# Performance work log

Measured on AMD Instinct MI355X. Metric: run time of the kernel, lower is better.

## Reference

```python
import jax, jax.numpy as jnp
import numpy as np

H, N, CH, L = 256, 256, 1, 1024


def setup_inputs() -> dict:
    key = jax.random.key(0)
    k1, k2, k3, k4 = jax.random.split(key, 4)
    # Hurwitz-like A so the discretized dA is stable (|eig| < 1) over L powers
    A = 0.05 * jax.random.normal(k1, (H, N, N), jnp.float32) - jnp.eye(N, dtype=jnp.float32)
    B = jax.random.normal(k2, (H, N), jnp.float32)
    C = jax.random.normal(k3, (CH, H, N), jnp.float32)
    log_dt = jax.random.uniform(k4, (H,), jnp.float32,
                                minval=np.log(1e-3), maxval=np.log(1e-1))
    return {"A": A, "B": B, "C": C, "log_dt": log_dt}


def reference(A, B, C, log_dt):
    # Bilinear (Tustin) discretization:
    #   dA = (I - dt/2 A)^{-1} (I + dt/2 A),  dB = dt * (I - dt/2 A)^{-1} B
    dt = jnp.exp(log_dt)                                   # (H,)
    I = jnp.eye(A.shape[-1], dtype=A.dtype)
    A_bwd = I - (dt[:, None, None] / 2) * A                # (H, N, N)
    A_fwd = I + (dt[:, None, None] / 2) * A                # (H, N, N)
    dB = dt[:, None] * jnp.linalg.solve(A_bwd, B[..., None])[..., 0]   # (H, N)
    dA = jnp.linalg.solve(A_bwd, A_fwd)                    # (H, N, N)

    # Krylov kernel: k[c,h,l] = C[c,h,:] @ dA^l @ dB[h,:]
    def step(x, _):
        y = jnp.einsum('chn,hn->ch', C, x)                 # contract with C
        x_next = jnp.einsum('hmn,hn->hm', dA, x)           # advance state
        return x_next, y

    _, ys = jax.lax.scan(step, dB, None, length=L)         # ys: (L, CH, H)
    k = jnp.transpose(ys, (1, 2, 0))                       # (CH, H, L)
    return k
```

## Files before the change

kernel.cpp:

```cpp
#include <hip/hip_runtime.h>
#include <cstdint>
#include <cstddef>

#define NH 256
#define ND 256
#define NL 1024
#define NUV 16
#define NWV 64

typedef __attribute__((ext_vector_type(4))) float f32x4;
typedef __attribute__((ext_vector_type(8))) short short8;
typedef __attribute__((ext_vector_type(8))) unsigned short u16x8;
typedef __attribute__((ext_vector_type(4))) unsigned short u16x4;
typedef __attribute__((ext_vector_type(4))) unsigned int u32x4;

__device__ __forceinline__ float bfrec(unsigned short hi, unsigned short lo) {
  return __uint_as_float(((unsigned)hi) << 16) + __uint_as_float(((unsigned)lo) << 16);
}
__device__ __forceinline__ unsigned rne16(unsigned u) {
  return u + 0x7FFFu + ((u >> 16) & 1u);
}
__device__ __forceinline__ void bfsplit(float x, unsigned short& hi, unsigned short& lo) {
  unsigned u = __float_as_uint(x);
  unsigned r1 = rne16(u);
  hi = (unsigned short)(r1 >> 16);
  float lf = x - __uint_as_float(r1 & 0xFFFF0000u);
  unsigned r2 = rne16(__float_as_uint(lf));
  lo = (unsigned short)(r2 >> 16);
}
__device__ __forceinline__ void gload16(const void* g, void* l) {
  __builtin_amdgcn_global_load_lds(
      (const __attribute__((address_space(1))) unsigned int*)g,
      (__attribute__((address_space(3))) unsigned int*)l, 16, 0, 0);
}
__device__ __forceinline__ int ksw(int row) { return (row >> 1) & 3; }

__global__ __launch_bounds__(256) void prep_kernel(
    const float* __restrict__ A, const float* __restrict__ log_dt,
    unsigned short* __restrict__ Mhi, unsigned short* __restrict__ Mlo)
{
  size_t e0 = ((size_t)blockIdx.x * 256 + threadIdx.x) * 16;
  int h = (int)(e0 >> 16);
  float hdt = 0.5f * __expf(log_dt[h]);
  unsigned short hb[16], lb[16];
#pragma unroll
  for (int i = 0; i < 4; ++i) {
    f32x4 v = *(const f32x4*)(A + e0 + i * 4);
#pragma unroll
    for (int j = 0; j < 4; ++j) bfsplit(v[j] * hdt, hb[i * 4 + j], lb[i * 4 + j]);
  }
  unsigned ph[8], pl[8];
#pragma unroll
  for (int i = 0; i < 8; ++i) {
    ph[i] = (unsigned)hb[2 * i] | ((unsigned)hb[2 * i + 1] << 16);
    pl[i] = (unsigned)lb[2 * i] | ((unsigned)lb[2 * i + 1] << 16);
  }
  u32x4 a0 = {ph[0], ph[1], ph[2], ph[3]}, a1 = {ph[4], ph[5], ph[6], ph[7]};
  u32x4 b0 = {pl[0], pl[1], pl[2], pl[3]}, b1 = {pl[4], pl[5], pl[6], pl[7]};
  *(u32x4*)(Mhi + e0) = a0; *(u32x4*)(Mhi + e0 + 8) = a1;
  *(u32x4*)(Mlo + e0) = b0; *(u32x4*)(Mlo + e0 + 8) = b1;
}

template <int YT, int ADDX, int OUTN, int OUTT, int QOUT>
__global__ __launch_bounds__(256) void gemm128_kernel(
    const unsigned short* __restrict__ Xhi, const unsigned short* __restrict__ Xlo,
    const unsigned short* __restrict__ Yhi, const unsigned short* __restrict__ Ylo,
    unsigned short* __restrict__ Dhi, unsigned short* __restrict__ Dlo,
    unsigned short* __restrict__ DThi, unsigned short* __restrict__ DTlo,
    unsigned short* __restrict__ Qhi, unsigned short* __restrict__ Qlo)
{
  __shared__ unsigned short lds[33792];
  int tid = threadIdx.x;
  int lane = tid & 63, w = tid >> 6;
  int bid = blockIdx.x;
  int h = bid & 255, part = bid >> 8;
  int m0 = (part >> 1) * 128, n0 = (part & 1) * 128;
  size_t mb = (size_t)h * 65536;

  f32x4 acc[2][8];
#pragma unroll
  for (int m = 0; m < 2; ++m)
#pragma unroll
    for (int n = 0; n < 8; ++n) { f32x4 z = {0.f, 0.f, 0.f, 0.f}; acc[m][n] = z; }

  auto STAGE = [&](int s, int kb) {
#pragma unroll
    for (int j = 0; j < 2; ++j) {
      int c = j * 256 + tid;
      if (YT) {
        int row = c >> 2, sp = c & 3;
        int koff = kb * 32 + ((sp ^ ksw(row)) << 3);
        size_t gx = mb + (size_t)(m0 + row) * 256 + koff;
        size_t gy = mb + (size_t)(n0 + row) * 256 + koff;
        gload16(Xhi + gx, &lds[s * 8192 + c * 8]);
        gload16(Xlo + gx, &lds[s * 8192 + 4096 + c * 8]);
        gload16(Yhi + gy, &lds[16384 + s * 8192 + c * 8]);
        gload16(Ylo + gy, &lds[16384 + s * 8192 + 4096 + c * 8]);
      } else {
        {
          int row = c >> 2, sp = c & 3;
          size_t go = mb + (size_t)(m0 + row) * 256 + kb * 32 + ((sp ^ ksw(row)) << 3);
          gload16(Xhi + go, &lds[s * 8192 + c * 8]);
          gload16(Xlo + go, &lds[s * 8192 + 4096 + c * 8]);
        }
        {
          int k = c >> 4, ns = c & 15;
          size_t go = mb + (size_t)(kb * 32 + k) * 256 + n0 + ns * 8;
          gload16(Yhi + go, &lds[16384 + s * 8192 + c * 8]);
          gload16(Ylo + go, &lds[16384 + s * 8192 + 4096 + c * 8]);
        }
      }
    }
  };

  STAGE(0, 0);
  __builtin_amdgcn_sched_barrier(0);

  int nn = tid & 127, kh = tid >> 7;
  int cur = 0;
  for (int kb = 0; kb < 8; ++kb) {
    int nxt = cur ^ 1;
    if (kb < 7) {
      STAGE(nxt, kb + 1);
      __builtin_amdgcn_sched_barrier(0);
      asm volatile("s_waitcnt vmcnt(8)" ::: "memory");
    } else {
      asm volatile("s_waitcnt vmcnt(0)" ::: "memory");
    }
    __builtin_amdgcn_sched_barrier(0);
    __builtin_amdgcn_s_barrier();
    __builtin_amdgcn_sched_barrier(0);

    unsigned short* yb = &lds[16384 + cur * 8192];
    if (!YT) {
      unsigned short rh[16], rl[16];
#pragma unroll
      for (int i = 0; i < 16; ++i) {
        rh[i] = yb[(kh * 16 + i) * 128 + nn];
        rl[i] = yb[4096 + (kh * 16 + i) * 128 + nn];
      }
      asm volatile("s_waitcnt lgkmcnt(0)" ::: "memory");
      __builtin_amdgcn_sched_barrier(0);
      __builtin_amdgcn_s_barrier();
      __builtin_amdgcn_sched_barrier(0);
#pragma unroll
      for (int s2 = 0; s2 < 2; ++s2) {
        int sl = kh * 2 + s2;
        int off = nn * 32 + ((sl ^ ksw(nn)) << 3);
        u16x8 vh, vl;
#pragma unroll
        for (int e = 0; e < 8; ++e) { vh[e] = rh[s2 * 8 + e]; vl[e] = rl[s2 * 8 + e]; }
        *(u16x8*)&yb[off] = vh;
        *(u16x8*)&yb[4096 + off] = vl;
      }
      asm volatile("s_waitcnt lgkmcnt(0)" ::: "memory");
      __builtin_amdgcn_sched_barrier(0);
      __builtin_amdgcn_s_barrier();
      __builtin_amdgcn_sched_barrier(0);
    }

    int kg = lane >> 4, li = lane & 15;
    const unsigned short* xb = &lds[cur * 8192];
    short8 bhi[8], blo[8];
#pragma unroll
    for (int n = 0; n < 8; ++n) {
      int rowN = n * 16 + li;
      int off = rowN * 32 + ((kg ^ ksw(rowN)) << 3);
      bhi[n] = *(const short8*)&yb[off];
      blo[n] = *(const short8*)&yb[4096 + off];
    }
    __builtin_amdgcn_s_setprio(1);
#pragma unroll
    for (int m = 0; m < 2; ++m) {
      int rowM = w * 32 + m * 16 + li;
      int off = rowM * 32 + ((kg ^ ksw(rowM)) << 3);
      short8 ahi = *(const short8*)&xb[off];
      short8 alo = *(const short8*)&xb[4096 + off];
#pragma unroll
      for (int n = 0; n < 8; ++n) {
        acc[m][n] = __builtin_amdgcn_mfma_f32_16x16x32_bf16(ahi, bhi[n], acc[m][n], 0, 0, 0);
        acc[m][n] = __builtin_amdgcn_mfma_f32_16x16x32_bf16(ahi, blo[n], acc[m][n], 0, 0, 0);
        acc[m][n] = __builtin_amdgcn_mfma_f32_16x16x32_bf16(alo, bhi[n], acc[m][n], 0, 0, 0);
      }
    }
    __builtin_amdgcn_s_setprio(0);
    __builtin_amdgcn_sched_barrier(0);
    __builtin_amdgcn_s_barrier();
    __builtin_amdgcn_sched_barrier(0);
    cur = nxt;
  }

  float* fb = (float*)lds;
  {
    int q0 = (lane >> 4) * 4, li = lane & 15;
#pragma unroll
    for (int m = 0; m < 2; ++m)
#pragma unroll
      for (int n = 0; n < 8; ++n)
#pragma unroll
        for (int q = 0; q < 4; ++q)
          fb[(w * 32 + m * 16 + q0 + q) * 132 + n * 16 + li] = acc[m][n][q];
  }
  __syncthreads();
  if (OUTN || ADDX) {
    int row = tid >> 1, half = tid & 1;
#pragma unroll 1
    for (int hp = 0; hp < 2; ++hp) {
      int c0 = half * 64 + hp * 32;
      float v[32];
#pragma unroll
      for (int u = 0; u < 8; ++u) {
        f32x4 t4 = *(const f32x4*)&fb[row * 132 + c0 + u * 4];
#pragma unroll
        for (int e = 0; e < 4; ++e) v[u * 4 + e] = t4[e];
      }
      size_t go = mb + (size_t)(m0 + row) * 256 + n0 + c0;
      float xv[32];
      if (ADDX || QOUT) {
#pragma unroll
        for (int u = 0; u < 4; ++u) {
          u16x8 xh = *(const u16x8*)(Xhi + go + u * 8);
          u16x8 xl = *(const u16x8*)(Xlo + go + u * 8);
#pragma unroll
          for (int e = 0; e < 8; ++e) xv[u * 8 + e] = bfrec(xh[e], xl[e]);
        }
        if (ADDX) {
#pragma unroll
          for (int e = 0; e < 32; ++e) v[e] += xv[e];
          if (OUTT) {
#pragma unroll
            for (int u = 0; u < 8; ++u) {
              f32x4 t4;
#pragma unroll
              for (int e = 0; e < 4; ++e) t4[e] = v[u * 4 + e];
              *(f32x4*)&fb[row * 132 + c0 + u * 4] = t4;
            }
          }
        }
      }
      if (OUTN) {
        unsigned hw[16], lw[16];
#pragma unroll
        for (int i = 0; i < 16; ++i) {
          unsigned short ha, la, hb2, lb2;
          bfsplit(v[2 * i], ha, la);
          bfsplit(v[2 * i + 1], hb2, lb2);
          hw[i] = (unsigned)ha | ((unsigned)hb2 << 16);
          lw[i] = (unsigned)la | ((unsigned)lb2 << 16);
        }
#pragma unroll
        for (int u = 0; u < 4; ++u) {
          u32x4 a = {hw[u * 4], hw[u * 4 + 1], hw[u * 4 + 2], hw[u * 4 + 3]};
          u32x4 b = {lw[u * 4], lw[u * 4 + 1], lw[u * 4 + 2], lw[u * 4 + 3]};
          *(u32x4*)(Dhi + go + u * 8) = a;
          *(u32x4*)(Dlo + go + u * 8) = b;
        }
      }
      if (QOUT) {
        int grow = m0 + row, gc0 = n0 + c0;
        float qv[32];
#pragma unroll
        for (int e = 0; e < 32; ++e)
          qv[e] = v[e] + 2.f * xv[e] + ((gc0 + e) == grow ? 1.f : 0.f);
        unsigned hw[16], lw[16];
#pragma unroll
        for (int i = 0; i < 16; ++i) {
          unsigned short ha, la, hb2, lb2;
          bfsplit(qv[2 * i], ha, la);
          bfsplit(qv[2 * i + 1], hb2, lb2);
          hw[i] = (unsigned)ha | ((unsigned)hb2 << 16);
          lw[i] = (unsigned)la | ((unsigned)lb2 << 16);
        }
#pragma unroll
        for (int u = 0; u < 4; ++u) {
          u32x4 a = {hw[u * 4], hw[u * 4 + 1], hw[u * 4 + 2], hw[u * 4 + 3]};
          u32x4 b = {lw[u * 4], lw[u * 4 + 1], lw[u * 4 + 2], lw[u * 4 + 3]};
          *(u32x4*)(Qhi + go + u * 8) = a;
          *(u32x4*)(Qlo + go + u * 8) = b;
        }
      }
    }
  }
  if (OUTT) {
    if (ADDX) __syncthreads();
    int c = tid & 127, rh2 = tid >> 7;
#pragma unroll 1
    for (int ch2 = 0; ch2 < 2; ++ch2) {
      int r0 = rh2 * 64 + ch2 * 32;
      float tv[32];
#pragma unroll
      for (int i = 0; i < 32; ++i) tv[i] = fb[(r0 + i) * 132 + c];
      unsigned hw[16], lw[16];
#pragma unroll
      for (int i = 0; i < 16; ++i) {
        unsigned short ha, la, hb2, lb2;
        bfsplit(tv[2 * i], ha, la);
        bfsplit(tv[2 * i + 1], hb2, lb2);
        hw[i] = (unsigned)ha | ((unsigned)hb2 << 16);
        lw[i] = (unsigned)la | ((unsigned)lb2 << 16);
      }
      size_t go = mb + (size_t)(n0 + c) * 256 + m0 + r0;
#pragma unroll
      for (int u = 0; u < 4; ++u) {
        u32x4 a = {hw[u * 4], hw[u * 4 + 1], hw[u * 4 + 2], hw[u * 4 + 3]};
        u32x4 b = {lw[u * 4], lw[u * 4 + 1], lw[u * 4 + 2], lw[u * 4 + 3]};
        *(u32x4*)(DThi + go + u * 8) = a;
        *(u32x4*)(DTlo + go + u * 8) = b;
      }
    }
  }
}

__global__ __launch_bounds__(256) void db_kernel(
    const unsigned short* __restrict__ dAhi, const unsigned short* __restrict__ dAlo,
    const float* __restrict__ Bv, const float* __restrict__ log_dt, float* __restrict__ dB)
{
  int h = blockIdx.x, r = threadIdx.x;
  __shared__ float bl[256];
  bl[r] = Bv[h * 256 + r];
  __syncthreads();
  const unsigned short* ph = dAhi + (size_t)h * 65536 + (size_t)r * 256;
  const unsigned short* pl = dAlo + (size_t)h * 65536 + (size_t)r * 256;
  float acc = bl[r];
  for (int c8 = 0; c8 < 32; ++c8) {
    u16x8 vh = *(const u16x8*)(ph + c8 * 8);
    u16x8 vl = *(const u16x8*)(pl + c8 * 8);
#pragma unroll
    for (int e = 0; e < 8; ++e) acc += bfrec(vh[e], vl[e]) * bl[c8 * 8 + e];
  }
  dB[h * 256 + r] = 0.5f * __expf(log_dt[h]) * acc;
}

__device__ __forceinline__ int physc(int c) { return c + ((c >> 4) << 2); }

__global__ __launch_bounds__(1024) void chainAB_kernel(
    const unsigned short* __restrict__ UTh, const unsigned short* __restrict__ UTl,
    const unsigned short* __restrict__ Gh, const unsigned short* __restrict__ Gl,
    const float* __restrict__ Cin, const float* __restrict__ dB,
    float* __restrict__ U, float* __restrict__ W, int base)
{
  int b = blockIdx.x + base;
  bool um = b < NH;
  int h = um ? b : b - NH;
  const unsigned short* mh = (um ? UTh : Gh) + (size_t)h * 65536;
  const unsigned short* ml = (um ? UTl : Gl) + (size_t)h * 65536;
  const float* x0 = um ? (Cin + (size_t)h * 256) : (dB + (size_t)h * 256);
  float* out = um ? (U + (size_t)h * (NUV * 256)) : (W + (size_t)h * (NWV * 256));
  int nv = um ? NUV : NWV;

  int tid = threadIdx.x;
  int rg = tid >> 4, cg = tid & 15;
  float mat[4][16];
#pragma unroll
  for (int rr = 0; rr < 4; ++rr) {
    const unsigned short* ph = mh + (size_t)(rg * 4 + rr) * 256 + cg * 16;
    const unsigned short* pl = ml + (size_t)(rg * 4 + rr) * 256 + cg * 16;
    u16x8 h0 = *(const u16x8*)ph, h1 = *(const u16x8*)(ph + 8);
    u16x8 l0 = *(const u16x8*)pl, l1 = *(const u16x8*)(pl + 8);
#pragma unroll
    for (int e = 0; e < 8; ++e) {
      mat[rr][e] = bfrec(h0[e], l0[e]);
      mat[rr][8 + e] = bfrec(h1[e], l1[e]);
    }
  }
  __shared__ float xb[2][320];
  if (tid < 256) {
    float vv = x0[tid];
    xb[0][physc(tid)] = vv;
    out[tid] = vv;
  }
  __syncthreads();
  int p = 0;
  for (int v = 1; v < nv; ++v) {
    float part[4] = {0.f, 0.f, 0.f, 0.f};
#pragma unroll
    for (int sl = 0; sl < 4; ++sl) {
      f32x4 xv = *(const f32x4*)&xb[p][cg * 20 + sl * 4];
#pragma unroll
      for (int rr = 0; rr < 4; ++rr)
#pragma unroll
        for (int e = 0; e < 4; ++e) part[rr] += mat[rr][sl * 4 + e] * xv[e];
    }
#pragma unroll
    for (int rr = 0; rr < 4; ++rr) {
      part[rr] += __shfl_xor(part[rr], 1, 64);
      part[rr] += __shfl_xor(part[rr], 2, 64);
      part[rr] += __shfl_xor(part[rr], 4, 64);
      part[rr] += __shfl_xor(part[rr], 8, 64);
    }
    float val = (cg == 0) ? part[0] : ((cg == 1) ? part[1] : ((cg == 2) ? part[2] : part[3]));
    if (cg < 4) {
      int row = rg * 4 + cg;
      xb[p ^ 1][physc(row)] = val;
      out[(size_t)v * 256 + row] = val;
    }
    __syncthreads();
    p ^= 1;
  }
}

__global__ __launch_bounds__(1024) void chainC_kernel(
    const unsigned short* __restrict__ dAhi, const unsigned short* __restrict__ dAlo,
    const unsigned short* __restrict__ Ghi, const unsigned short* __restrict__ Glo,
    const float* __restrict__ Cin, const float* __restrict__ dB,
    float* __restrict__ U, float* __restrict__ W)
{
  int b = blockIdx.x;
  bool um = b < NH;
  int h = um ? b : b - NH;
  const float* x0 = um ? (Cin + (size_t)h * 256) : (dB + (size_t)h * 256);
  float* out = um ? (U + (size_t)h * (NUV * 256)) : (W + (size_t)h * (NWV * 256));
  int nv = um ? NUV : NWV;

  int tid = threadIdx.x;
  int rg = tid >> 4, cg = tid & 15;
  float mat[4][16];
  if (um) {
    const unsigned short* mh = dAhi + (size_t)h * 65536;
    const unsigned short* ml = dAlo + (size_t)h * 65536;
#pragma unroll
    for (int j = 0; j < 16; ++j) {
      u16x4 h4 = *(const u16x4*)(mh + (size_t)(cg * 16 + j) * 256 + rg * 4);
      u16x4 l4 = *(const u16x4*)(ml + (size_t)(cg * 16 + j) * 256 + rg * 4);
#pragma unroll
      for (int rr = 0; rr < 4; ++rr) mat[rr][j] = bfrec(h4[rr], l4[rr]);
    }
  } else {
    const unsigned short* mh = Ghi + (size_t)h * 65536;
    const unsigned short* ml = Glo + (size_t)h * 65536;
#pragma unroll
    for (int rr = 0; rr < 4; ++rr) {
      const unsigned short* ph = mh + (size_t)(rg * 4 + rr) * 256 + cg * 16;
      const unsigned short* pl = ml + (size_t)(rg * 4 + rr) * 256 + cg * 16;
      u16x8 h0 = *(const u16x8*)ph, h1 = *(const u16x8*)(ph + 8);
      u16x8 l0 = *(const u16x8*)pl, l1 = *(const u16x8*)(pl + 8);
#pragma unroll
      for (int e = 0; e < 8; ++e) {
        mat[rr][e] = bfrec(h0[e], l0[e]);
        mat[rr][8 + e] = bfrec(h1[e], l1[e]);
      }
    }
  }
  __shared__ float xb[2][320];
  if (tid < 256) {
    float vv = x0[tid];
    xb[0][physc(tid)] = vv;
    out[tid] = vv;
  }
  __syncthreads();
  int p = 0;
  for (int v = 1; v < nv; ++v) {
    float part[4] = {0.f, 0.f, 0.f, 0.f};
#pragma unroll
    for (int sl = 0; sl < 4; ++sl) {
      f32x4 xv = *(const f32x4*)&xb[p][cg * 20 + sl * 4];
#pragma unroll
      for (int rr = 0; rr < 4; ++rr)
#pragma unroll
        for (int e = 0; e < 4; ++e) part[rr] += mat[rr][sl * 4 + e] * xv[e];
    }
#pragma unroll
    for (int rr = 0; rr < 4; ++rr) {
      part[rr] += __shfl_xor(part[rr], 1, 64);
      part[rr] += __shfl_xor(part[rr], 2, 64);
      part[rr] += __shfl_xor(part[rr], 4, 64);
      part[rr] += __shfl_xor(part[rr], 8, 64);
    }
    float val = (cg == 0) ? part[0] : ((cg == 1) ? part[1] : ((cg == 2) ? part[2] : part[3]));
    if (cg < 4) {
      int row = rg * 4 + cg;
      xb[p ^ 1][physc(row)] = val;
      out[(size_t)v * 256 + row] = val;
    }
    __syncthreads();
    p ^= 1;
  }
}

__global__ __launch_bounds__(512) void gram_kernel(
    const float* __restrict__ U, const float* __restrict__ W, float* __restrict__ out)
{
  int b = blockIdx.x;
  int h = b >> 1, jh = b & 1;
  __shared__ float ul[16][260];
  __shared__ float wl[32][260];
  int tid = threadIdx.x;
  const float* Up = U + (size_t)h * (NUV * 256);
  const float* Wp = W + (size_t)h * (NWV * 256) + (size_t)jh * 32 * 256;
  {
    int r = tid >> 5, cb = (tid & 31) * 8;
    f32x4 a = *(const f32x4*)(Up + (size_t)r * 256 + cb);
    f32x4 c2 = *(const f32x4*)(Up + (size_t)r * 256 + cb + 4);
    *(f32x4*)&ul[r][cb] = a;
    *(f32x4*)&ul[r][cb + 4] = c2;
  }
  {
    int r = tid >> 4, cb = (tid & 15) * 16;
#pragma unroll
    for (int u = 0; u < 4; ++u) {
      f32x4 a = *(const f32x4*)(Wp + (size_t)r * 256 + cb + u * 4);
      *(f32x4*)&wl[r][cb + u * 4] = a;
    }
  }
  __syncthreads();
  int i = tid >> 5, j2 = tid & 31;
  float acc = 0.f;
#pragma unroll 8
  for (int c = 0; c < 256; c += 4) {
    f32x4 uu = *(const f32x4*)&ul[i][c];
    f32x4 ww = *(const f32x4*)&wl[j2][c];
    acc += uu[0] * ww[0] + uu[1] * ww[1] + uu[2] * ww[2] + uu[3] * ww[3];
  }
  out[(size_t)h * 1024 + (size_t)(jh * 32 + j2) * 16 + i] = acc;
}

__global__ void bail_kernel(float* out, unsigned mib) {
  if (threadIdx.x == 0) out[blockIdx.x] = -(2.0e6f + (float)mib * 4096.0f);
}

extern "C" void kernel_launch(void* const* d_in, const int* in_sizes, int n_in,
                              void* d_out, int out_size, void* d_ws, size_t ws_size,
                              hipStream_t stream) {
  const float* A = (const float*)d_in[0];
  const float* B = (const float*)d_in[1];
  const float* C = (const float*)d_in[2];
  const float* log_dt = (const float*)d_in[3];
  float* out = (float*)d_out;

  const size_t PLANE = (size_t)NH * ND * ND * 2;
  const size_t PHALF = (size_t)NH * ND * ND;
  const size_t VEC = (size_t)NH * ND * 4;
  const size_t USZ = (size_t)NH * NUV * ND * 4;
  const size_t WSZ = (size_t)NH * NWV * ND * 4;
  const size_t EXTRA = VEC + USZ + WSZ;
  const size_t NEED_A = 10 * PLANE + EXTRA;
  const size_t NEED_B = 8 * PLANE + EXTRA;
  const size_t NEED_C = 6 * PLANE + EXTRA;
  if (ws_size < NEED_C) {
    bail_kernel<<<8, 64, 0, stream>>>(out, (unsigned)(ws_size >> 20));
    return;
  }
  uint8_t* w8 = (uint8_t*)d_ws;
  auto P = [&](int i) -> unsigned short* { return (unsigned short*)(w8 + (size_t)i * PLANE); };

  if (ws_size >= NEED_B) {
    bool tierA = (ws_size >= NEED_A);
    int np = tierA ? 10 : 8;
    float* dBp = (float*)(w8 + (size_t)np * PLANE);
    float* Up = (float*)(w8 + (size_t)np * PLANE + VEC);
    float* Wp = (float*)(w8 + (size_t)np * PLANE + VEC + USZ);
    prep_kernel<<<4096, 256, 0, stream>>>(A, log_dt, P(0), P(1));
    if (tierA) {
      gemm128_kernel<0, 0, 1, 1, 1><<<1024, 256, 0, stream>>>(
          P(0), P(1), P(0), P(1), P(2), P(3), P(4), P(5), P(6), P(7));
      gemm128_kernel<1, 1, 1, 0, 0><<<1024, 256, 0, stream>>>(
          P(6), P(7), P(4), P(5), P(8), P(9), nullptr, nullptr, nullptr, nullptr);
      gemm128_kernel<1, 0, 0, 1, 0><<<1024, 256, 0, stream>>>(
          P(2), P(3), P(4), P(5), nullptr, nullptr, P(0), P(1), nullptr, nullptr);
      gemm128_kernel<1, 1, 1, 1, 0><<<1024, 256, 0, stream>>>(
          P(8), P(9), P(0), P(1), P(2), P(3), P(4), P(5), nullptr, nullptr);
      db_kernel<<<NH, 256, 0, stream>>>(P(2), P(3), B, log_dt, dBp);
      gemm128_kernel<1, 0, 1, 1, 0><<<1024, 256, 0, stream>>>(
          P(2), P(3), P(4), P(5), P(6), P(7), P(8), P(9), nullptr, nullptr);
      gemm128_kernel<1, 0, 1, 1, 0><<<1024, 256, 0, stream>>>(
          P(6), P(7), P(8), P(9), P(0), P(1), P(2), P(3), nullptr, nullptr);
      gemm128_kernel<1, 0, 1, 1, 0><<<1024, 256, 0, stream>>>(
          P(0), P(1), P(2), P(3), P(6), P(7), P(8), P(9), nullptr, nullptr);
      gemm128_kernel<1, 0, 1, 0, 0><<<1024, 256, 0, stream>>>(
          P(6), P(7), P(8), P(9), P(0), P(1), nullptr, nullptr, nullptr, nullptr);
      chainAB_kernel<<<2 * NH, 1024, 0, stream>>>(P(4), P(5), P(0), P(1), C, dBp, Up, Wp, 0);
    } else {
      gemm128_kernel<0, 0, 1, 1, 1><<<1024, 256, 0, stream>>>(
          P(0), P(1), P(0), P(1), P(2), P(3), P(4), P(5), P(6), P(7));
      gemm128_kernel<1, 1, 1, 0, 0><<<1024, 256, 0, stream>>>(
          P(6), P(7), P(4), P(5), P(0), P(1), nullptr, nullptr, nullptr, nullptr);
      gemm128_kernel<1, 0, 0, 1, 0><<<1024, 256, 0, stream>>>(
          P(2), P(3), P(4), P(5), nullptr, nullptr, P(6), P(7), nullptr, nullptr);
      gemm128_kernel<1, 1, 1, 1, 0><<<1024, 256, 0, stream>>>(
          P(0), P(1), P(6), P(7), P(2), P(3), P(4), P(5), nullptr, nullptr);
      db_kernel<<<NH, 256, 0, stream>>>(P(2), P(3), B, log_dt, dBp);
      chainAB_kernel<<<NH, 1024, 0, stream>>>(P(4), P(5), P(4), P(5), C, dBp, Up, Wp, 0);
      gemm128_kernel<1, 0, 1, 1, 0><<<1024, 256, 0, stream>>>(
          P(2), P(3), P(4), P(5), P(0), P(1), P(6), P(7), nullptr, nullptr);
      gemm128_kernel<1, 0, 1, 1, 0><<<1024, 256, 0, stream>>>(
          P(0), P(1), P(6), P(7), P(2), P(3), P(4), P(5), nullptr, nullptr);
      gemm128_kernel<1, 0, 1, 1, 0><<<1024, 256, 0, stream>>>(
          P(2), P(3), P(4), P(5), P(0), P(1), P(6), P(7), nullptr, nullptr);
      gemm128_kernel<1, 0, 1, 0, 0><<<1024, 256, 0, stream>>>(
          P(0), P(1), P(6), P(7), P(2), P(3), nullptr, nullptr, nullptr, nullptr);
      chainAB_kernel<<<NH, 1024, 0, stream>>>(P(2), P(3), P(2), P(3), C, dBp, Up, Wp, NH);
    }
    gram_kernel<<<2 * NH, 512, 0, stream>>>(Up, Wp, out);
  } else {
    float* dBp = (float*)(w8 + 6 * PLANE);
    float* Up = (float*)(w8 + 6 * PLANE + VEC);
    float* Wp = (float*)(w8 + 6 * PLANE + VEC + USZ);
    auto HI = [&](int b2) -> unsigned short* { return P(2 * b2); };
    auto LO = [&](int b2) -> unsigned short* { return P(2 * b2) + PHALF; };
    prep_kernel<<<4096, 256, 0, stream>>>(A, log_dt, HI(0), LO(0));
    gemm128_kernel<0, 0, 1, 0, 1><<<1024, 256, 0, stream>>>(
        HI(0), LO(0), HI(0), LO(0), HI(1), LO(1), nullptr, nullptr, HI(2), LO(2));
    gemm128_kernel<0, 1, 1, 0, 0><<<1024, 256, 0, stream>>>(
        HI(2), LO(2), HI(1), LO(1), HI(0), LO(0), nullptr, nullptr, nullptr, nullptr);
    gemm128_kernel<0, 0, 1, 0, 0><<<1024, 256, 0, stream>>>(
        HI(1), LO(1), HI(1), LO(1), HI(2), LO(2), nullptr, nullptr, nullptr, nullptr);
    gemm128_kernel<0, 1, 1, 0, 0><<<1024, 256, 0, stream>>>(
        HI(0), LO(0), HI(2), LO(2), HI(1), LO(1), nullptr, nullptr, nullptr, nullptr);
    db_kernel<<<NH, 256, 0, stream>>>(HI(1), LO(1), B, log_dt, dBp);
    gemm128_kernel<0, 0, 1, 0, 0><<<1024, 256, 0, stream>>>(
        HI(1), LO(1), HI(1), LO(1), HI(0), LO(0), nullptr, nullptr, nullptr, nullptr);
    gemm128_kernel<0, 0, 1, 0, 0><<<1024, 256, 0, stream>>>(
        HI(0), LO(0), HI(0), LO(0), HI(2), LO(2), nullptr, nullptr, nullptr, nullptr);
    gemm128_kernel<0, 0, 1, 0, 0><<<1024, 256, 0, stream>>>(
        HI(2), LO(2), HI(2), LO(2), HI(0), LO(0), nullptr, nullptr, nullptr, nullptr);
    gemm128_kernel<0, 0, 1, 0, 0><<<1024, 256, 0, stream>>>(
        HI(0), LO(0), HI(0), LO(0), HI(2), LO(2), nullptr, nullptr, nullptr, nullptr);
    chainC_kernel<<<2 * NH, 1024, 0, stream>>>(HI(1), LO(1), HI(2), LO(2), C, dBp, Up, Wp);
    gram_kernel<<<2 * NH, 512, 0, stream>>>(Up, Wp, out);
  }
}
```

Measured before the change: 650.9 us.

## Restructure Neumann/inverse GEMM chain with fused transpose prep and axpy kernel

Replaces the tiered 8/10-plane schedule with a single 8-plane path. A new prep kernel writes both the scaled A split and its transpose through an LDS tile. A new elementwise axpy3 kernel forms 2M+M^2+I directly, where a GEMM with add used to do it. The GEMM sequence is reordered to build the inverse and the dA powers with a different set of products, likely fewer or cheaper ones. This adds two small bandwidth-bound kernels and changes numerical ordering, which could affect accuracy.

Measured after the change: 774.7 us. +19.0%, slower.

```diff
diff --git a/kernel.cpp b/kernel.cpp
--- a/kernel.cpp
+++ b/kernel.cpp
@@ -59,6 +59,99 @@
   u32x4 b0 = {pl[0], pl[1], pl[2], pl[3]}, b1 = {pl[4], pl[5], pl[6], pl[7]};
   *(u32x4*)(Mhi + e0) = a0; *(u32x4*)(Mhi + e0 + 8) = a1;
   *(u32x4*)(Mlo + e0) = b0; *(u32x4*)(Mlo + e0 + 8) = b1;
+}
+
+__global__ __launch_bounds__(256) void prepT_kernel(
+    const float* __restrict__ A, const float* __restrict__ log_dt,
+    unsigned short* __restrict__ Mhi, unsigned short* __restrict__ Mlo,
+    unsigned short* __restrict__ Thi, unsigned short* __restrict__ Tlo)
+{
+  int h = blockIdx.x >> 4, tile = blockIdx.x & 15;
+  int r0 = (tile >> 2) * 64, c0 = (tile & 3) * 64;
+  float hdt = 0.5f * __expf(log_dt[h]);
+  __shared__ unsigned t[64][65];
+  int tid = threadIdx.x;
+  int r = tid >> 2, cq = tid & 3;
+  size_t base = (size_t)h * 65536;
+  const float* Ap = A + base + (size_t)(r0 + r) * 256 + c0 + cq * 16;
+  unsigned short hb[16], lb[16];
+#pragma unroll
+  for (int i = 0; i < 4; ++i) {
+    f32x4 v = *(const f32x4*)(Ap + i * 4);
+#pragma unroll
+    for (int j = 0; j < 4; ++j) bfsplit(v[j] * hdt, hb[i * 4 + j], lb[i * 4 + j]);
+  }
+  {
+    unsigned ph[8], pl[8];
+#pragma unroll
+    for (int i = 0; i < 8; ++i) {
+      ph[i] = (unsigned)hb[2 * i] | ((unsigned)hb[2 * i + 1] << 16);
+      pl[i] = (unsigned)lb[2 * i] | ((unsigned)lb[2 * i + 1] << 16);
+    }
+    size_t go = base + (size_t)(r0 + r) * 256 + c0 + cq * 16;
+    u32x4 a0 = {ph[0], ph[1], ph[2], ph[3]}, a1 = {ph[4], ph[5], ph[6], ph[7]};
+    u32x4 b0 = {pl[0], pl[1], pl[2], pl[3]}, b1 = {pl[4], pl[5], pl[6], pl[7]};
+    *(u32x4*)(Mhi + go) = a0; *(u32x4*)(Mhi + go + 8) = a1;
+    *(u32x4*)(Mlo + go) = b0; *(u32x4*)(Mlo + go + 8) = b1;
+  }
+#pragma unroll
+  for (int i = 0; i < 16; ++i) t[r][cq * 16 + i] = ((unsigned)hb[i] << 16) | lb[i];
+  __syncthreads();
+  int c = tid >> 2, rq = tid & 3;
+  unsigned short hbT[16], lbT[16];
+#pragma unroll
+  for (int i = 0; i < 16; ++i) {
+    unsigned wv = t[rq * 16 + i][c];
+    hbT[i] = (unsigned short)(wv >> 16);
+    lbT[i] = (unsigned short)(wv & 0xFFFFu);
+  }
+  {
+    unsigned ph[8], pl[8];
+#pragma unroll
+    for (int i = 0; i < 8; ++i) {
+      ph[i] = (unsigned)hbT[2 * i] | ((unsigned)hbT[2 * i + 1] << 16);
+      pl[i] = (unsigned)lbT[2 * i] | ((unsigned)lbT[2 * i + 1] << 16);
+    }
+    size_t go = base + (size_t)(c0 + c) * 256 + r0 + rq * 16;
+    u32x4 a0 = {ph[0], ph[1], ph[2], ph[3]}, a1 = {ph[4], ph[5], ph[6], ph[7]};
+    u32x4 b0 = {pl[0], pl[1], pl[2], pl[3]}, b1 = {pl[4], pl[5], pl[6], pl[7]};
+    *(u32x4*)(Thi + go) = a0; *(u32x4*)(Thi + go + 8) = a1;
+    *(u32x4*)(Tlo + go) = b0; *(u32x4*)(Tlo + go + 8) = b1;
+  }
+}
+
+__global__ __launch_bounds__(256) void axpy3_kernel(
+    const unsigned short* __restrict__ Mhi, const unsigned short* __restrict__ Mlo,
+    const unsigned short* __restrict__ T1hi, const unsigned short* __restrict__ T1lo,
+    unsigned short* __restrict__ Qhi, unsigned short* __restrict__ Qlo)
+{
+  size_t e0 = ((size_t)blockIdx.x * 256 + threadIdx.x) * 8;
+  u16x8 mh = *(const u16x8*)(Mhi + e0);
+  u16x8 ml = *(const u16x8*)(Mlo + e0);
+  u16x8 th = *(const u16x8*)(T1hi + e0);
+  u16x8 tl = *(const u16x8*)(T1lo + e0);
+  int idx = (int)(e0 & 65535);
+  int r = idx >> 8, cb = idx & 255;
+  float vv[8];
+#pragma unroll
+  for (int e = 0; e < 8; ++e) {
+    float q = 2.f * bfrec(mh[e], ml[e]) + bfrec(th[e], tl[e]);
+    if ((cb + e) == r) q += 1.f;
+    vv[e] = q;
+  }
+  unsigned hw[4], lw[4];
+#pragma unroll
+  for (int i = 0; i < 4; ++i) {
+    unsigned short ha, la, hb2, lb2;
+    bfsplit(vv[2 * i], ha, la);
+    bfsplit(vv[2 * i + 1], hb2, lb2);
+    hw[i] = (unsigned)ha | ((unsigned)hb2 << 16);
+    lw[i] = (unsigned)la | ((unsigned)lb2 << 16);
+  }
+  u32x4 a = {hw[0], hw[1], hw[2], hw[3]};
+  u32x4 b = {lw[0], lw[1], lw[2], lw[3]};
+  *(u32x4*)(Qhi + e0) = a;
+  *(u32x4*)(Qlo + e0) = b;
 }
 
 template <int YT, int ADDX, int OUTN, int OUTT, int QOUT>
@@ -533,8 +626,7 @@
   const size_t USZ = (size_t)NH * NUV * ND * 4;
   const size_t WSZ = (size_t)NH * NWV * ND * 4;
   const size_t EXTRA = VEC + USZ + WSZ;
-  const size_t NEED_A = 10 * PLANE + EXTRA;
-  const size_t NEED_B = 8 * PLANE + EXTRA;
+  const size_t NEED_T8 = 8 * PLANE;
   const size_t NEED_C = 6 * PLANE + EXTRA;
   if (ws_size < NEED_C) {
     bail_kernel<<<8, 64, 0, stream>>>(out, (unsigned)(ws_size >> 20));
@@ -543,53 +635,31 @@
   uint8_t* w8 = (uint8_t*)d_ws;
   auto P = [&](int i) -> unsigned short* { return (unsigned short*)(w8 + (size_t)i * PLANE); };
 
-  if (ws_size >= NEED_B) {
-    bool tierA = (ws_size >= NEED_A);
-    int np = tierA ? 10 : 8;
-    float* dBp = (float*)(w8 + (size_t)np * PLANE);
-    float* Up = (float*)(w8 + (size_t)np * PLANE + VEC);
-    float* Wp = (float*)(w8 + (size_t)np * PLANE + VEC + USZ);
-    prep_kernel<<<4096, 256, 0, stream>>>(A, log_dt, P(0), P(1));
-    if (tierA) {
-      gemm128_kernel<0, 0, 1, 1, 1><<<1024, 256, 0, stream>>>(
-          P(0), P(1), P(0), P(1), P(2), P(3), P(4), P(5), P(6), P(7));
-      gemm128_kernel<1, 1, 1, 0, 0><<<1024, 256, 0, stream>>>(
-          P(6), P(7), P(4), P(5), P(8), P(9), nullptr, nullptr, nullptr, nullptr);
-      gemm128_kernel<1, 0, 0, 1, 0><<<1024, 256, 0, stream>>>(
-          P(2), P(3), P(4), P(5), nullptr, nullptr, P(0), P(1), nullptr, nullptr);
-      gemm128_kernel<1, 1, 1, 1, 0><<<1024, 256, 0, stream>>>(
-          P(8), P(9), P(0), P(1), P(2), P(3), P(4), P(5), nullptr, nullptr);
-      db_kernel<<<NH, 256, 0, stream>>>(P(2), P(3), B, log_dt, dBp);
-      gemm128_kernel<1, 0, 1, 1, 0><<<1024, 256, 0, stream>>>(
-          P(2), P(3), P(4), P(5), P(6), P(7), P(8), P(9), nullptr, nullptr);
-      gemm128_kernel<1, 0, 1, 1, 0><<<1024, 256, 0, stream>>>(
-          P(6), P(7), P(8), P(9), P(0), P(1), P(2), P(3), nullptr, nullptr);
-      gemm128_kernel<1, 0, 1, 1, 0><<<1024, 256, 0, stream>>>(
-          P(0), P(1), P(2), P(3), P(6), P(7), P(8), P(9), nullptr, nullptr);
-      gemm128_kernel<1, 0, 1, 0, 0><<<1024, 256, 0, stream>>>(
-          P(6), P(7), P(8), P(9), P(0), P(1), nullptr, nullptr, nullptr, nullptr);
-      chainAB_kernel<<<2 * NH, 1024, 0, stream>>>(P(4), P(5), P(0), P(1), C, dBp, Up, Wp, 0);
-    } else {
-      gemm128_kernel<0, 0, 1, 1, 1><<<1024, 256, 0, stream>>>(
-          P(0), P(1), P(0), P(1), P(2), P(3), P(4), P(5), P(6), P(7));
-      gemm128_kernel<1, 1, 1, 0, 0><<<1024, 256, 0, stream>>>(
-          P(6), P(7), P(4), P(5), P(0), P(1), nullptr, nullptr, nullptr, nullptr);
-      gemm128_kernel<1, 0, 0, 1, 0><<<1024, 256, 0, stream>>>(
-          P(2), P(3), P(4), P(5), nullptr, nullptr, P(6), P(7), nullptr, nullptr);
-      gemm128_kernel<1, 1, 1, 1, 0><<<1024, 256, 0, stream>>>(
-          P(0), P(1), P(6), P(7), P(2), P(3), P(4), P(5), nullptr, nullptr);
-      db_kernel<<<NH, 256, 0, stream>>>(P(2), P(3), B, log_dt, dBp);
-      chainAB_kernel<<<NH, 1024, 0, stream>>>(P(4), P(5), P(4), P(5), C, dBp, Up, Wp, 0);
-      gemm128_kernel<1, 0, 1, 1, 0><<<1024, 256, 0, stream>>>(
-          P(2), P(3), P(4), P(5), P(0), P(1), P(6), P(7), nullptr, nullptr);
-      gemm128_kernel<1, 0, 1, 1, 0><<<1024, 256, 0, stream>>>(
-          P(0), P(1), P(6), P(7), P(2), P(3), P(4), P(5), nullptr, nullptr);
-      gemm128_kernel<1, 0, 1, 1, 0><<<1024, 256, 0, stream>>>(
-          P(2), P(3), P(4), P(5), P(0), P(1), P(6), P(7), nullptr, nullptr);
-      gemm128_kernel<1, 0, 1, 0, 0><<<1024, 256, 0, stream>>>(
-          P(0), P(1), P(6), P(7), P(2), P(3), nullptr, nullptr, nullptr, nullptr);
-      chainAB_kernel<<<NH, 1024, 0, stream>>>(P(2), P(3), P(2), P(3), C, dBp, Up, Wp, NH);
-    }
+  if (ws_size >= NEED_T8) {
+    float* dBp = (float*)(w8 + 4 * PLANE);
+    float* Up = (float*)(w8 + 4 * PLANE + VEC);
+    float* Wp = (float*)(w8 + 4 * PLANE + VEC + USZ);
+    prepT_kernel<<<NH * 16, 256, 0, stream>>>(A, log_dt, P(0), P(1), P(2), P(3));
+    gemm128_kernel<1, 0, 1, 1, 0><<<1024, 256, 0, stream>>>(
+        P(0), P(1), P(2), P(3), P(4), P(5), P(6), P(7), nullptr, nullptr);
+    axpy3_kernel<<<8192, 256, 0, stream>>>(P(0), P(1), P(4), P(5), P(2), P(3));
+    gemm128_kernel<1, 0, 0, 1, 0><<<1024, 256, 0, stream>>>(
+        P(4), P(5), P(6), P(7), nullptr, nullptr, P(0), P(1), nullptr, nullptr);
+    gemm128_kernel<1, 1, 1, 0, 0><<<1024, 256, 0, stream>>>(
+        P(2), P(3), P(6), P(7), P(4), P(5), nullptr, nullptr, nullptr, nullptr);
+    gemm128_kernel<1, 1, 1, 1, 0><<<1024, 256, 0, stream>>>(
+        P(4), P(5), P(0), P(1), P(2), P(3), P(6), P(7), nullptr, nullptr);
+    db_kernel<<<NH, 256, 0, stream>>>(P(2), P(3), B, log_dt, dBp);
+    chainAB_kernel<<<NH, 1024, 0, stream>>>(P(6), P(7), P(6), P(7), C, dBp, Up, Wp, 0);
+    gemm128_kernel<1, 0, 1, 0, 0><<<1024, 256, 0, stream>>>(
+        P(2), P(3), P(6), P(7), P(0), P(1), nullptr, nullptr, nullptr, nullptr);
+    gemm128_kernel<0, 0, 1, 1, 0><<<1024, 256, 0, stream>>>(
+        P(0), P(1), P(0), P(1), P(2), P(3), P(6), P(7), nullptr, nullptr);
+    gemm128_kernel<1, 0, 1, 0, 0><<<1024, 256, 0, stream>>>(
+        P(2), P(3), P(6), P(7), P(0), P(1), nullptr, nullptr, nullptr, nullptr);
+    gemm128_kernel<0, 0, 1, 0, 0><<<1024, 256, 0, stream>>>(
+        P(0), P(1), P(0), P(1), P(2), P(3), nullptr, nullptr, nullptr, nullptr);
+    chainAB_kernel<<<NH, 1024, 0, stream>>>(P(2), P(3), P(2), P(3), C, dBp, Up, Wp, NH);
     gram_kernel<<<2 * NH, 512, 0, stream>>>(Up, Wp, out);
   } else {
     float* dBp = (float*)(w8 + 6 * PLANE);
```
